# Optimization experiments

Measured on AMD Instinct MI355X. Metric: run time of the kernel, lower is better.

Reference implementation:

```python
import jax, jax.numpy as jnp
import numpy as np

V, B, E, H, T = 32000, 64, 64, 256, 32


def setup_inputs() -> dict:
    key = jax.random.key(0)
    ks = jax.random.split(key, 16)
    n = lambda k, shape, s: (jax.random.normal(k, shape, jnp.float32) * s)
    return {
        "input_x": jax.random.randint(ks[0], (B, T), 0, V, dtype=jnp.int32),
        "given_num": 16,
        "start_token": jnp.zeros((B,), jnp.int32),
        "g_embeddings": n(ks[1], (V, E), 0.1),
        "Wi": n(ks[2], (E, H), 0.1), "Ui": n(ks[3], (H, H), 0.1), "bi": jnp.zeros((H,), jnp.float32),
        "Wf": n(ks[4], (E, H), 0.1), "Uf": n(ks[5], (H, H), 0.1), "bf": jnp.zeros((H,), jnp.float32),
        "Wog": n(ks[6], (E, H), 0.1), "Uog": n(ks[7], (H, H), 0.1), "bog": jnp.zeros((H,), jnp.float32),
        "Wc": n(ks[8], (E, H), 0.1), "Uc": n(ks[9], (H, H), 0.1), "bc": jnp.zeros((H,), jnp.float32),
        "Wo": n(ks[10], (H, V), 0.05), "bo": jnp.zeros((V,), jnp.float32),
    }


def reference(input_x, given_num, start_token, g_embeddings,
              Wi, Ui, bi, Wf, Uf, bf, Wog, Uog, bog, Wc, Uc, bc, Wo, bo):
    Bsz, Tlen = input_x.shape
    Hdim = Ui.shape[0]
    emb_x = g_embeddings[input_x]                 # [B,T,E] teacher embeddings
    x0 = g_embeddings[start_token]                # [B,E]
    h0 = jnp.zeros((Bsz, Hdim), g_embeddings.dtype)
    c0 = jnp.zeros((Bsz, Hdim), g_embeddings.dtype)

    def step(carry, scan_in):
        x_t, h, c = carry
        t, teacher_tok, teacher_emb = scan_in
        i_g = jax.nn.sigmoid(x_t @ Wi + h @ Ui + bi)
        f_g = jax.nn.sigmoid(x_t @ Wf + h @ Uf + bf)
        o_g = jax.nn.sigmoid(x_t @ Wog + h @ Uog + bog)
        c_hat = jnp.tanh(x_t @ Wc + h @ Uc + bc)
        c_new = f_g * c + i_g * c_hat
        h_new = o_g * jnp.tanh(c_new)
        logits = h_new @ Wo + bo                  # [B,V]
        # original: argmax over Multinomial(logits=log_softmax).probs == argmax(logits)
        sampled = jnp.argmax(logits, axis=-1).astype(jnp.int32)
        teach = t < given_num                     # scalar bool for this step
        tok = jnp.where(teach, teacher_tok, sampled)
        x_next = jnp.where(teach, teacher_emb, g_embeddings[sampled])
        return (x_next, h_new, c_new), tok

    scan_in = (jnp.arange(Tlen), input_x.T, jnp.transpose(emb_x, (1, 0, 2)))
    _, toks = jax.lax.scan(step, (x0, h0, c0), scan_in)
    return toks.T                                 # [B,T] int32, matches gen_x
```

## Files before the change

kernel.cpp:

```cpp
#include <hip/hip_runtime.h>
#include <math.h>
#include <stdint.h>

#define Bz 64
#define Tz 32
#define Ez 64
#define Hz 256
#define Vz 32000
#define KTOT 320

typedef unsigned long long u64;
typedef unsigned int u32;

__device__ __forceinline__ u32 map_f32(float f) {
  u32 u = __float_as_uint(f);
  return (u & 0x80000000u) ? ~u : (u | 0x80000000u);
}

__device__ __forceinline__ void gload_lds16(const float* g, float* l) {
  __builtin_amdgcn_global_load_lds(
      (const __attribute__((address_space(1))) void*)g,
      (__attribute__((address_space(3))) void*)l, 16, 0, 0);
}

__global__ void k_prep(const float* __restrict__ Wi, const float* __restrict__ Ui,
                       const float* __restrict__ Wf, const float* __restrict__ Uf,
                       const float* __restrict__ Wog, const float* __restrict__ Uog,
                       const float* __restrict__ Wc, const float* __restrict__ Uc,
                       float* __restrict__ P4, u64* __restrict__ key) {
  int j = blockIdx.x;
  int k = threadIdx.x;
  float g0, g1, g2, g3;
  if (k < Ez) {
    g0 = Wi[k*Hz + j]; g1 = Wf[k*Hz + j]; g2 = Wog[k*Hz + j]; g3 = Wc[k*Hz + j];
  } else {
    int kk = k - Ez;
    g0 = Ui[kk*Hz + j]; g1 = Uf[kk*Hz + j]; g2 = Uog[kk*Hz + j]; g3 = Uc[kk*Hz + j];
  }
  float* p = P4 + ((size_t)j*KTOT + k)*4;
  p[0] = g0; p[1] = g1; p[2] = g2; p[3] = g3;
  if (j == 0 && k < 2*Bz) key[k] = 0ull;
}

__global__ __launch_bounds__(512) void k_gates(
    int t, const int* __restrict__ gnp,
    const int* __restrict__ input_x, const int* __restrict__ start_tok,
    const float* __restrict__ emb, const float* __restrict__ P4,
    const float* __restrict__ bi_, const float* __restrict__ bf_,
    const float* __restrict__ bog_, const float* __restrict__ bc_,
    const float* __restrict__ hT_in, float* __restrict__ hT_out,
    float* __restrict__ cT,
    const u64* __restrict__ key_prev, u64* __restrict__ key_cur,
    int* __restrict__ out) {
  extern __shared__ float sm[];
  float* xh = sm;
  float* pw = sm + 20480;
  float* sc = sm + 25600;
  int*   tok_s = (int*)(sm + 26624);

  int tid = threadIdx.x;
  int blk = blockIdx.x;
  int gn = *gnp;

  if (tid < Bz) {
    int b = tid, tk;
    if (t == 0)          tk = start_tok[b];
    else if (t - 1 < gn) tk = input_x[b*Tz + (t-1)];
    else                 tk = (int)(~(u32)(key_prev[b] & 0xFFFFFFFFull));
    tok_s[b] = tk;
    if (blk == 0 && t > 0) out[b*Tz + (t-1)] = tk;
  }
  if (blk == 0 && tid >= 64 && tid < 64 + Bz) key_cur[tid - 64] = 0ull;
  __syncthreads();

  {
    int b = tid & 63, part = tid >> 6;
    const float4* e4 = (const float4*)(emb + (size_t)tok_s[b]*Ez + part*8);
    float4 v0 = e4[0], v1 = e4[1];
    int k0 = part*8;
    xh[(k0+0)*Bz + b] = v0.x; xh[(k0+1)*Bz + b] = v0.y;
    xh[(k0+2)*Bz + b] = v0.z; xh[(k0+3)*Bz + b] = v0.w;
    xh[(k0+4)*Bz + b] = v1.x; xh[(k0+5)*Bz + b] = v1.y;
    xh[(k0+6)*Bz + b] = v1.z; xh[(k0+7)*Bz + b] = v1.w;
  }
  if (t > 0) {
    const float4* s4 = (const float4*)hT_in;
    float4* d4 = (float4*)(xh + Ez*Bz);
    #pragma unroll
    for (int i = 0; i < 8; ++i) d4[tid + i*512] = s4[tid + i*512];
  }
  {
    const float* psrc = P4 + (size_t)blk*5120;
    #pragma unroll
    for (int i = 0; i < 10; ++i) pw[tid + i*512] = psrc[tid + i*512];
  }
  __syncthreads();

  int wid = tid >> 6, lane = tid & 63;
  int j4 = wid >> 1, seg = wid & 1;
  int j = blk*4 + j4;
  const float* wrow = pw + j4*1280;
  int kbeg = seg ? 160 : 0;
  int kend = (t > 0) ? (seg ? 320 : 160) : (seg ? 0 : 64);

  float ai = 0.f, af = 0.f, ao = 0.f, ac = 0.f;
  #pragma unroll 2
  for (int k = kbeg; k < kend; k += 4) {
    #pragma unroll
    for (int kk = 0; kk < 4; ++kk) {
      float4 wv = *(const float4*)(wrow + (k+kk)*4);
      float xv = xh[(k+kk)*Bz + lane];
      ai = fmaf(xv, wv.x, ai); af = fmaf(xv, wv.y, af);
      ao = fmaf(xv, wv.z, ao); ac = fmaf(xv, wv.w, ac);
    }
  }

  if (seg == 1) {
    sc[j4*256 +   0 + lane] = ai;
    sc[j4*256 +  64 + lane] = af;
    sc[j4*256 + 128 + lane] = ao;
    sc[j4*256 + 192 + lane] = ac;
  }
  __syncthreads();
  if (seg == 0) {
    ai += sc[j4*256 +   0 + lane] + bi_[j];
    af += sc[j4*256 +  64 + lane] + bf_[j];
    ao += sc[j4*256 + 128 + lane] + bog_[j];
    ac += sc[j4*256 + 192 + lane] + bc_[j];
    float gi = 1.f/(1.f + expf(-ai));
    float gf = 1.f/(1.f + expf(-af));
    float go = 1.f/(1.f + expf(-ao));
    float gc = tanhf(ac);
    float cold = (t > 0) ? cT[j*Bz + lane] : 0.f;
    float cn = gf*cold + gi*gc;
    float hn = go * tanhf(cn);
    cT[j*Bz + lane]     = cn;
    hT_out[j*Bz + lane] = hn;
  }
}

__global__ __launch_bounds__(512, 1) void k_logits(
    int t, const int* __restrict__ gnp,
    const float* __restrict__ hT,
    const float* __restrict__ Wo, const float* __restrict__ bo,
    u64* __restrict__ key_cur) {
  int gn = *gnp;
  if (t < gn) return;
  extern __shared__ float sm[];
  float* hLDS = sm;
  float* wbuf = sm + 16384;

  int tid = threadIdx.x;
  int bid = blockIdx.x;
  int wid = tid >> 6, lane = tid & 63;
  int seg = wid >> 1, chalf = wid & 1;
  int rg = lane >> 3, cg = lane & 7;

  float bo8[8];
  {
    const float4* b4 = (const float4*)(bo + bid*128 + chalf*64 + cg*8);
    float4 x = b4[0], y = b4[1];
    bo8[0]=x.x; bo8[1]=x.y; bo8[2]=x.z; bo8[3]=x.w;
    bo8[4]=y.x; bo8[5]=y.y; bo8[6]=y.z; bo8[7]=y.w;
  }
  {
    const float4* s4 = (const float4*)hT;
    float4* d4 = (float4*)hLDS;
    #pragma unroll
    for (int i = 0; i < 8; ++i) d4[tid + i*512] = s4[tid + i*512];
  }
  __syncthreads();

  float acc[8][8] = {};
  float* wb = wbuf + wid*2048;
  const float* gW = Wo + bid*128;

#define STAGE(q_, p_) { \
    int kb = seg*64 + (q_)*8; \
    _Pragma("unroll") \
    for (int i = 0; i < 4; ++i) { \
      int row = kb + i*2 + (lane>>5); \
      gload_lds16(gW + (size_t)row*Vz + ((lane&31)<<2), wb + (p_)*1024 + i*256); \
    } }

#define COMPUTE(q_, p_) { \
    const float* wp = wb + (p_)*1024; \
    const float* hp = hLDS + (seg*64 + (q_)*8)*Bz + rg*8; \
    _Pragma("unroll") \
    for (int kk = 0; kk < 8; ++kk) { \
      float4 h0 = *(const float4*)(hp + kk*Bz); \
      float4 h1 = *(const float4*)(hp + kk*Bz + 4); \
      float4 w0 = *(const float4*)(wp + kk*128 + chalf*64 + cg*8); \
      float4 w1 = *(const float4*)(wp + kk*128 + chalf*64 + cg*8 + 4); \
      float hv[8] = {h0.x,h0.y,h0.z,h0.w,h1.x,h1.y,h1.z,h1.w}; \
      float wv[8] = {w0.x,w0.y,w0.z,w0.w,w1.x,w1.y,w1.z,w1.w}; \
      _Pragma("unroll") \
      for (int r = 0; r < 8; ++r) { \
        _Pragma("unroll") \
        for (int c = 0; c < 8; ++c) acc[r][c] = fmaf(hv[r], wv[c], acc[r][c]); } \
    } }

  STAGE(0, 0)
  #pragma unroll 1
  for (int q = 0; q < 7; ++q) {
    STAGE(q+1, (q+1)&1)
    asm volatile("s_waitcnt vmcnt(4)" ::: "memory");
    __builtin_amdgcn_sched_barrier(0);
    COMPUTE(q, q&1)
  }
  asm volatile("s_waitcnt vmcnt(0)" ::: "memory");
  __builtin_amdgcn_sched_barrier(0);
  COMPUTE(7, 1)
#undef STAGE
#undef COMPUTE

  float* scratch = wbuf;
  __syncthreads();
  if (wid >= 4) {
    float* r = scratch + (wid-4)*4096;
    #pragma unroll
    for (int i = 0; i < 64; ++i) r[i*64 + lane] = acc[i>>3][i&7];
  }
  __syncthreads();
  if (wid < 4) {
    const float* r = scratch + wid*4096;
    #pragma unroll
    for (int i = 0; i < 64; ++i) acc[i>>3][i&7] += r[i*64 + lane];
  }
  __syncthreads();
  if (wid == 2 || wid == 3) {
    float* r = scratch + (wid-2)*4096;
    #pragma unroll
    for (int i = 0; i < 64; ++i) r[i*64 + lane] = acc[i>>3][i&7];
  }
  __syncthreads();

  if (wid < 2) {
    const float* r = scratch + wid*4096;
    #pragma unroll
    for (int i = 0; i < 64; ++i) acc[i>>3][i&7] += r[i*64 + lane];

    int cbase = bid*128 + chalf*64 + cg*8;
    float myv = 0.f; int myi = 0;
    #pragma unroll
    for (int rr = 0; rr < 8; ++rr) {
      float bv = acc[rr][0] + bo8[0]; int bix = cbase;
      #pragma unroll
      for (int c = 1; c < 8; ++c) {
        float v = acc[rr][c] + bo8[c];
        if (v > bv) { bv = v; bix = cbase + c; }
      }
      #pragma unroll
      for (int m = 1; m < 8; m <<= 1) {
        float ov = __shfl_xor(bv, m, 64);
        int   oi = __shfl_xor(bix, m, 64);
        if (ov > bv || (ov == bv && oi < bix)) { bv = ov; bix = oi; }
      }
      if (cg == rr) { myv = bv; myi = bix; }
    }
    int row = rg*8 + cg;
    u64 kv = ((u64)map_f32(myv) << 32) | (u32)(~(u32)myi);
    atomicMax(&key_cur[row], kv);
  }
}

__global__ void k_final(const int* __restrict__ gnp, const int* __restrict__ input_x,
                        const u64* __restrict__ key_last, int* __restrict__ out) {
  int b = threadIdx.x;
  int gn = *gnp;
  int tk;
  if (Tz - 1 < gn) tk = input_x[b*Tz + Tz - 1];
  else             tk = (int)(~(u32)(key_last[b] & 0xFFFFFFFFull));
  out[b*Tz + Tz - 1] = tk;
}

extern "C" void kernel_launch(void* const* d_in, const int* in_sizes, int n_in,
                              void* d_out, int out_size, void* d_ws, size_t ws_size,
                              hipStream_t stream) {
  const int*   input_x   = (const int*)d_in[0];
  const int*   gnp       = (const int*)d_in[1];
  const int*   start_tok = (const int*)d_in[2];
  const float* emb = (const float*)d_in[3];
  const float* Wi  = (const float*)d_in[4];
  const float* Ui  = (const float*)d_in[5];
  const float* bi  = (const float*)d_in[6];
  const float* Wf  = (const float*)d_in[7];
  const float* Uf  = (const float*)d_in[8];
  const float* bff = (const float*)d_in[9];
  const float* Wog = (const float*)d_in[10];
  const float* Uog = (const float*)d_in[11];
  const float* bog = (const float*)d_in[12];
  const float* Wc  = (const float*)d_in[13];
  const float* Uc  = (const float*)d_in[14];
  const float* bc  = (const float*)d_in[15];
  const float* Wo  = (const float*)d_in[16];
  const float* bo  = (const float*)d_in[17];
  int* out = (int*)d_out;

  float* wsf = (float*)d_ws;
  float* hTA = wsf;
  float* hTB = wsf + 16384;
  float* cT  = wsf + 32768;
  u64*   key = (u64*)(wsf + 49152);
  float* P4  = wsf + 49152 + 256;

  size_t gsm = (size_t)(20480 + 5120 + 1024 + 64) * 4;
  size_t lsm = (size_t)(16384 + 16384) * 4;
  hipFuncSetAttribute((const void*)k_gates,
                      hipFuncAttributeMaxDynamicSharedMemorySize, (int)gsm);
  hipFuncSetAttribute((const void*)k_logits,
                      hipFuncAttributeMaxDynamicSharedMemorySize, (int)lsm);

  k_prep<<<dim3(256), dim3(320), 0, stream>>>(Wi, Ui, Wf, Uf, Wog, Uog, Wc, Uc, P4, key);

  for (int t = 0; t < Tz; ++t) {
    const float* hT_in  = (t & 1) ? hTA : hTB;
    float*       hT_out = (t & 1) ? hTB : hTA;
    const u64* key_prev = key + ((t + 1) & 1) * Bz;
    u64*       key_cur  = key + (t & 1) * Bz;
    k_gates<<<dim3(64), dim3(512), gsm, stream>>>(
        t, gnp, input_x, start_tok, emb, P4, bi, bff, bog, bc,
        hT_in, hT_out, cT, key_prev, key_cur, out);
    k_logits<<<dim3(250), dim3(512), lsm, stream>>>(
        t, gnp, hT_out, Wo, bo, key_cur);
  }
  k_final<<<dim3(1), dim3(64), 0, stream>>>(
      gnp, input_x, key + ((Tz - 1) & 1) * Bz, out);
}
```

Baseline: 731.3 us.

## Score logits in bf16, then rescore a candidate shortlist exactly in fp32

Converts Wo to a bf16 copy once per call and runs the per-step vocabulary projection on bf16 weights and hidden state. Any column within an error bound of the running row max (0.02·|h|·max|w|) goes into a per-row candidate list. A new k_pick kernel rescores those candidates exactly in fp32 and takes the argmax, with ties going to the lower index. The aim is to halve weight traffic in the dominant logits pass. In exchange it adds a Wo conversion pass per call, an extra launch per step, and atomics for the list. Correctness depends on the list caps (2048 entries, 128 rescored) not overflowing. The new path runs only when the workspace is large enough.

```diff
diff --git a/kernel.cpp b/kernel.cpp
--- a/kernel.cpp
+++ b/kernel.cpp
@@ -8,28 +8,43 @@
 #define Hz 256
 #define Vz 32000
 #define KTOT 320
+#define LCAP 2048
+#define THRC 0.02f
 
 typedef unsigned long long u64;
 typedef unsigned int u32;
+typedef unsigned short u16;
 
 __device__ __forceinline__ u32 map_f32(float f) {
   u32 u = __float_as_uint(f);
   return (u & 0x80000000u) ? ~u : (u | 0x80000000u);
 }
-
+__device__ __forceinline__ float unmap_f32(u32 u) {
+  return __uint_as_float((u & 0x80000000u) ? (u & 0x7FFFFFFFu) : ~u);
+}
+__device__ __forceinline__ u16 f2bf(float f) {
+  u32 u = __float_as_uint(f);
+  return (u16)((u + 0x7FFFu + ((u >> 16) & 1u)) >> 16);
+}
 __device__ __forceinline__ void gload_lds16(const float* g, float* l) {
   __builtin_amdgcn_global_load_lds(
       (const __attribute__((address_space(1))) void*)g,
       (__attribute__((address_space(3))) void*)l, 16, 0, 0);
 }
+__device__ __forceinline__ void gload_lds16u(const u16* g, u16* l) {
+  __builtin_amdgcn_global_load_lds(
+      (const __attribute__((address_space(1))) void*)g,
+      (__attribute__((address_space(3))) void*)l, 16, 0, 0);
+}
 
 __global__ void k_prep(const float* __restrict__ Wi, const float* __restrict__ Ui,
                        const float* __restrict__ Wf, const float* __restrict__ Uf,
                        const float* __restrict__ Wog, const float* __restrict__ Uog,
                        const float* __restrict__ Wc, const float* __restrict__ Uc,
-                       float* __restrict__ P4, u64* __restrict__ key) {
-  int j = blockIdx.x;
-  int k = threadIdx.x;
+                       float* __restrict__ P4, u64* __restrict__ key,
+                       int* __restrict__ cnt, u32* __restrict__ gmax,
+                       u32* __restrict__ wn2) {
+  int j = blockIdx.x, k = threadIdx.x;
   float g0, g1, g2, g3;
   if (k < Ez) {
     g0 = Wi[k*Hz + j]; g1 = Wf[k*Hz + j]; g2 = Wog[k*Hz + j]; g3 = Wc[k*Hz + j];
@@ -40,6 +55,36 @@
   float* p = P4 + ((size_t)j*KTOT + k)*4;
   p[0] = g0; p[1] = g1; p[2] = g2; p[3] = g3;
   if (j == 0 && k < 2*Bz) key[k] = 0ull;
+  if (j == 1 && k < Bz)   cnt[k] = 0;
+  if (j == 2 && k < Bz)   gmax[k] = 0u;
+  if (j == 3 && k == 0)   *wn2 = 0u;
+}
+
+__global__ __launch_bounds__(512) void wb_prep(const float* __restrict__ Wo,
+                                               u16* __restrict__ Wb,
+                                               u32* __restrict__ wn2) {
+  __shared__ float cnorm[128];
+  int bid = blockIdx.x, tid = threadIdx.x;
+  const float* src = Wo + bid*128;
+  u16* dst = Wb + (size_t)bid*32768;
+  for (int idx = tid; idx < 32768; idx += 512) {
+    int k = idx >> 7, c = idx & 127;
+    dst[idx] = f2bf(src[(size_t)k*Vz + c]);
+  }
+  if (tid < 128) {
+    float s = 0.f;
+    for (int k = 0; k < Hz; ++k) {
+      float w = src[(size_t)k*Vz + tid];
+      s = fmaf(w, w, s);
+    }
+    cnorm[tid] = s;
+  }
+  __syncthreads();
+  if (tid == 0) {
+    float m = cnorm[0];
+    for (int i = 1; i < 128; ++i) m = fmaxf(m, cnorm[i]);
+    atomicMax(wn2, map_f32(m));
+  }
 }
 
 __global__ __launch_bounds__(512) void k_gates(
@@ -49,8 +94,9 @@
     const float* __restrict__ bi_, const float* __restrict__ bf_,
     const float* __restrict__ bog_, const float* __restrict__ bc_,
     const float* __restrict__ hT_in, float* __restrict__ hT_out,
-    float* __restrict__ cT,
+    u16* __restrict__ hTb_out, float* __restrict__ cT,
     const u64* __restrict__ key_prev, u64* __restrict__ key_cur,
+    const int* __restrict__ tokp, int mode,
     int* __restrict__ out) {
   extern __shared__ float sm[];
   float* xh = sm;
@@ -66,7 +112,8 @@
     int b = tid, tk;
     if (t == 0)          tk = start_tok[b];
     else if (t - 1 < gn) tk = input_x[b*Tz + (t-1)];
-    else                 tk = (int)(~(u32)(key_prev[b] & 0xFFFFFFFFull));
+    else                 tk = mode ? tokp[b]
+                              : (int)(~(u32)(key_prev[b] & 0xFFFFFFFFull));
     tok_s[b] = tk;
     if (blk == 0 && t > 0) out[b*Tz + (t-1)] = tk;
   }
@@ -134,12 +181,253 @@
     float cold = (t > 0) ? cT[j*Bz + lane] : 0.f;
     float cn = gf*cold + gi*gc;
     float hn = go * tanhf(cn);
-    cT[j*Bz + lane]     = cn;
-    hT_out[j*Bz + lane] = hn;
-  }
-}
-
-__global__ __launch_bounds__(512, 1) void k_logits(
+    cT[j*Bz + lane]       = cn;
+    hT_out[j*Bz + lane]   = hn;
+    hTb_out[j*Bz + lane]  = f2bf(hn);
+  }
+}
+
+__global__ __launch_bounds__(512, 1) void k_logits_b(
+    int t, const int* __restrict__ gnp,
+    const u16* __restrict__ hTb,
+    const u16* __restrict__ Wb,
+    const float* __restrict__ bo,
+    const u32* __restrict__ wn2p, float* __restrict__ rn2_g,
+    u32* __restrict__ gmax,
+    u64* __restrict__ list, int* __restrict__ cnt) {
+  int gn = *gnp;
+  if (t < gn) return;
+  extern __shared__ float sm[];
+  u16* hLDSb = (u16*)sm;
+  u16* wbuf  = (u16*)sm + 16384;
+  float* rnp  = sm + 12288;
+  float* rn2l = sm + 12800;
+
+  int tid = threadIdx.x;
+  int bid = blockIdx.x;
+  int wid = tid >> 6, lane = tid & 63;
+  int seg = wid >> 1, chalf = wid & 1;
+  int rg = lane >> 3, cg = lane & 7;
+
+  float wn = sqrtf(unmap_f32(*wn2p));
+
+  float bo8[8];
+  {
+    const float4* b4 = (const float4*)(bo + bid*128 + chalf*64 + cg*8);
+    float4 x = b4[0], y = b4[1];
+    bo8[0]=x.x; bo8[1]=x.y; bo8[2]=x.z; bo8[3]=x.w;
+    bo8[4]=y.x; bo8[5]=y.y; bo8[6]=y.z; bo8[7]=y.w;
+  }
+  {
+    const uint4* s4 = (const uint4*)hTb;
+    uint4* d4 = (uint4*)hLDSb;
+    #pragma unroll
+    for (int i = 0; i < 4; ++i) d4[tid + i*512] = s4[tid + i*512];
+  }
+  __syncthreads();
+
+  {
+    int b = tid & 63, part = tid >> 6;
+    float s = 0.f;
+    #pragma unroll 8
+    for (int k = part*32; k < part*32 + 32; ++k) {
+      float v = __uint_as_float((u32)hLDSb[k*Bz + b] << 16);
+      s = fmaf(v, v, s);
+    }
+    rnp[part*64 + b] = s;
+  }
+  __syncthreads();
+  if (tid < 64) {
+    float s = 0.f;
+    #pragma unroll
+    for (int p = 0; p < 8; ++p) s += rnp[p*64 + tid];
+    rn2l[tid] = s;
+    rn2_g[tid] = s;
+  }
+  __syncthreads();
+
+  float thr8[8];
+  if (wid < 2) {
+    #pragma unroll
+    for (int rr = 0; rr < 8; ++rr)
+      thr8[rr] = THRC * sqrtf(rn2l[rg*8 + rr]) * wn;
+  }
+
+  float acc[8][8] = {};
+  u16* wb = wbuf + wid*1024;
+  const u16* gW = Wb + (size_t)bid*32768 + chalf*64 + (lane & 7)*8
+                + (size_t)(seg*64 + (lane >> 3))*128;
+
+#define STAGE(q_, s_) gload_lds16u(gW + (size_t)(q_)*8*128, wb + (s_)*512);
+
+#define COMPUTE(q_, s_) { \
+    const u16* wp = wb + (s_)*512; \
+    const u16* hp = hLDSb + (seg*64 + (q_)*8)*Bz + rg*8; \
+    _Pragma("unroll") \
+    for (int kk = 0; kk < 8; ++kk) { \
+      uint4 hq = *(const uint4*)(hp + kk*Bz); \
+      uint4 wq = *(const uint4*)(wp + kk*64 + cg*8); \
+      float hv[8], wv[8]; \
+      hv[0]=__uint_as_float(hq.x<<16); hv[1]=__uint_as_float(hq.x&0xFFFF0000u); \
+      hv[2]=__uint_as_float(hq.y<<16); hv[3]=__uint_as_float(hq.y&0xFFFF0000u); \
+      hv[4]=__uint_as_float(hq.z<<16); hv[5]=__uint_as_float(hq.z&0xFFFF0000u); \
+      hv[6]=__uint_as_float(hq.w<<16); hv[7]=__uint_as_float(hq.w&0xFFFF0000u); \
+      wv[0]=__uint_as_float(wq.x<<16); wv[1]=__uint_as_float(wq.x&0xFFFF0000u); \
+      wv[2]=__uint_as_float(wq.y<<16); wv[3]=__uint_as_float(wq.y&0xFFFF0000u); \
+      wv[4]=__uint_as_float(wq.z<<16); wv[5]=__uint_as_float(wq.z&0xFFFF0000u); \
+      wv[6]=__uint_as_float(wq.w<<16); wv[7]=__uint_as_float(wq.w&0xFFFF0000u); \
+      _Pragma("unroll") \
+      for (int r = 0; r < 8; ++r) { \
+        _Pragma("unroll") \
+        for (int c = 0; c < 8; ++c) acc[r][c] = fmaf(hv[r], wv[c], acc[r][c]); } \
+    } }
+
+  STAGE(0, 0)
+  #pragma unroll 1
+  for (int q = 0; q < 7; ++q) {
+    STAGE(q+1, (q+1)&1)
+    asm volatile("s_waitcnt vmcnt(1)" ::: "memory");
+    __builtin_amdgcn_sched_barrier(0);
+    COMPUTE(q, q&1)
+  }
+  asm volatile("s_waitcnt vmcnt(0)" ::: "memory");
+  __builtin_amdgcn_sched_barrier(0);
+  COMPUTE(7, 1)
+#undef STAGE
+#undef COMPUTE
+
+  float* scratch = sm;
+  __syncthreads();
+  if (wid >= 4) {
+    float* r = scratch + (wid-4)*4096;
+    #pragma unroll
+    for (int i = 0; i < 64; ++i) r[i*64 + lane] = acc[i>>3][i&7];
+  }
+  __syncthreads();
+  if (wid < 4) {
+    const float* r = scratch + wid*4096;
+    #pragma unroll
+    for (int i = 0; i < 64; ++i) acc[i>>3][i&7] += r[i*64 + lane];
+  }
+  __syncthreads();
+  if (wid == 2 || wid == 3) {
+    float* r = scratch + (wid-2)*4096;
+    #pragma unroll
+    for (int i = 0; i < 64; ++i) r[i*64 + lane] = acc[i>>3][i&7];
+  }
+  __syncthreads();
+
+  if (wid < 2) {
+    const float* r = scratch + wid*4096;
+    #pragma unroll
+    for (int i = 0; i < 64; ++i) acc[i>>3][i&7] += r[i*64 + lane];
+
+    int cbase = bid*128 + chalf*64 + cg*8;
+    #pragma unroll
+    for (int rr = 0; rr < 8; ++rr) {
+      float bv = acc[rr][0] + bo8[0];
+      #pragma unroll
+      for (int c = 1; c < 8; ++c) bv = fmaxf(bv, acc[rr][c] + bo8[c]);
+      #pragma unroll
+      for (int m = 1; m < 8; m <<= 1) bv = fmaxf(bv, __shfl_xor(bv, m, 64));
+      int row = rg*8 + rr;
+      float cur = 0.f;
+      if (cg == 0) {
+        u32 old = atomicMax(&gmax[row], map_f32(bv));
+        cur = fmaxf(unmap_f32(old), bv);
+      }
+      float thrw = __shfl(cur, rg*8, 64) - thr8[rr];
+      #pragma unroll
+      for (int c = 0; c < 8; ++c) {
+        float v = acc[rr][c] + bo8[c];
+        if (v >= thrw) {
+          int idx = atomicAdd(&cnt[row], 1);
+          if (idx < LCAP)
+            list[(size_t)row*LCAP + idx] =
+                ((u64)map_f32(v) << 32) | (u32)(~(u32)(cbase + c));
+        }
+      }
+    }
+  }
+}
+
+__global__ __launch_bounds__(256) void k_pick(
+    int t, const int* __restrict__ gnp,
+    const float* __restrict__ hT,
+    const float* __restrict__ Wo, const float* __restrict__ bo,
+    const u32* __restrict__ wn2p, const float* __restrict__ rn2_g,
+    u64* __restrict__ list, int* __restrict__ cnt, u32* __restrict__ gmax,
+    int* __restrict__ tok) {
+  int gn = *gnp;
+  if (t < gn) return;
+  int b = blockIdx.x, tid = threadIdx.x;
+  __shared__ u64 smax[4];
+  __shared__ u64 sbest[4];
+  __shared__ int scol[128];
+  __shared__ int scnt;
+
+  float wn = sqrtf(unmap_f32(*wn2p));
+  float thrb = THRC * sqrtf(rn2_g[b]) * wn;
+
+  int n = cnt[b]; if (n > LCAP) n = LCAP;
+  const u64* L = list + (size_t)b*LCAP;
+  if (tid == 0) scnt = 0;
+
+  u64 m = 0;
+  for (int i = tid; i < n; i += 256) { u64 v = L[i]; if (v > m) m = v; }
+  #pragma unroll
+  for (int s = 1; s < 64; s <<= 1) {
+    u64 o = __shfl_xor(m, s, 64);
+    if (o > m) m = o;
+  }
+  if ((tid & 63) == 0) smax[tid >> 6] = m;
+  __syncthreads();
+  u64 gm = smax[0];
+  #pragma unroll
+  for (int s = 1; s < 4; ++s) if (smax[s] > gm) gm = smax[s];
+  float thr = unmap_f32((u32)(gm >> 32)) - thrb;
+
+  for (int i = tid; i < n; i += 256) {
+    u64 v = L[i];
+    if (unmap_f32((u32)(v >> 32)) >= thr) {
+      int s = atomicAdd(&scnt, 1);
+      if (s < 128) scol[s] = (int)(~(u32)(v & 0xFFFFFFFFull));
+    }
+  }
+  __syncthreads();
+  int ns = scnt < 128 ? scnt : 128;
+
+  int w = tid >> 6, lane = tid & 63;
+  float bestv = -3.4e38f; int bestc = 0x7FFFFFFF;
+  for (int base = 0; base < ns; base += 4) {
+    int ci = base + w;
+    if (ci < ns) {
+      int c = scol[ci];
+      int k0 = lane*4;
+      float pv = 0.f;
+      #pragma unroll
+      for (int i = 0; i < 4; ++i)
+        pv = fmaf(hT[(k0+i)*Bz + b], Wo[(size_t)(k0+i)*Vz + c], pv);
+      #pragma unroll
+      for (int s = 1; s < 64; s <<= 1) pv += __shfl_xor(pv, s, 64);
+      pv += bo[c];
+      if (pv > bestv || (pv == bestv && c < bestc)) { bestv = pv; bestc = c; }
+    }
+  }
+  if (lane == 0)
+    sbest[w] = ((u64)map_f32(bestv) << 32) | (u32)(~(u32)bestc);
+  __syncthreads();
+  if (tid == 0) {
+    u64 bb = sbest[0];
+    #pragma unroll
+    for (int s = 1; s < 4; ++s) if (sbest[s] > bb) bb = sbest[s];
+    tok[b]  = (int)(~(u32)(bb & 0xFFFFFFFFull));
+    cnt[b]  = 0;
+    gmax[b] = 0u;
+  }
+}
+
+__global__ __launch_bounds__(512, 1) void k_logits_f32(
     int t, const int* __restrict__ gnp,
     const float* __restrict__ hT,
     const float* __restrict__ Wo, const float* __restrict__ bo,
@@ -265,12 +553,14 @@
 }
 
 __global__ void k_final(const int* __restrict__ gnp, const int* __restrict__ input_x,
-                        const u64* __restrict__ key_last, int* __restrict__ out) {
+                        const u64* __restrict__ key_last, const int* __restrict__ tokp,
+                        int mode, int* __restrict__ out) {
   int b = threadIdx.x;
   int gn = *gnp;
   int tk;
   if (Tz - 1 < gn) tk = input_x[b*Tz + Tz - 1];
-  else             tk = (int)(~(u32)(key_last[b] & 0xFFFFFFFFull));
+  else             tk = mode ? tokp[b]
+                        : (int)(~(u32)(key_last[b] & 0xFFFFFFFFull));
   out[b*Tz + Tz - 1] = tk;
 }
 
@@ -297,21 +587,37 @@
   const float* bo  = (const float*)d_in[17];
   int* out = (int*)d_out;
 
-  float* wsf = (float*)d_ws;
-  float* hTA = wsf;
-  float* hTB = wsf + 16384;
-  float* cT  = wsf + 32768;
-  u64*   key = (u64*)(wsf + 49152);
-  float* P4  = wsf + 49152 + 256;
-
-  size_t gsm = (size_t)(20480 + 5120 + 1024 + 64) * 4;
-  size_t lsm = (size_t)(16384 + 16384) * 4;
+  float* wsf  = (float*)d_ws;
+  float* hTA  = wsf;
+  float* hTB  = wsf + 16384;
+  float* cT   = wsf + 32768;
+  u64*   key  = (u64*)(wsf + 49152);
+  int*   tok  = (int*)(wsf + 49408);
+  int*   cnt  = (int*)(wsf + 49472);
+  u32*   gmax = (u32*)(wsf + 49536);
+  float* rn2g = wsf + 49600;
+  u32*   wn2  = (u32*)(wsf + 49664);
+  u16*   hTb  = (u16*)(wsf + 49728);
+  float* P4   = wsf + 57920;
+  u64*   list = (u64*)(wsf + 385600);
+  u16*   Wb   = (u16*)(wsf + 647744);
+
+  int mode = ws_size >= (size_t)(647744 + 4096000) * 4;
+
+  size_t gsm  = (size_t)(20480 + 5120 + 1024 + 64) * 4;
+  size_t lsmB = 65536;
+  size_t lsmF = (size_t)(16384 + 16384) * 4;
   hipFuncSetAttribute((const void*)k_gates,
                       hipFuncAttributeMaxDynamicSharedMemorySize, (int)gsm);
-  hipFuncSetAttribute((const void*)k_logits,
-                      hipFuncAttributeMaxDynamicSharedMemorySize, (int)lsm);
-
-  k_prep<<<dim3(256), dim3(320), 0, stream>>>(Wi, Ui, Wf, Uf, Wog, Uog, Wc, Uc, P4, key);
+  hipFuncSetAttribute((const void*)k_logits_b,
+                      hipFuncAttributeMaxDynamicSharedMemorySize, (int)lsmB);
+  hipFuncSetAttribute((const void*)k_logits_f32,
+                      hipFuncAttributeMaxDynamicSharedMemorySize, (int)lsmF);
+
+  k_prep<<<dim3(256), dim3(320), 0, stream>>>(Wi, Ui, Wf, Uf, Wog, Uog, Wc, Uc,
+                                              P4, key, cnt, gmax, wn2);
+  if (mode)
+    wb_prep<<<dim3(250), dim3(512), 0, stream>>>(Wo, Wb, wn2);
 
   for (int t = 0; t < Tz; ++t) {
     const float* hT_in  = (t & 1) ? hTA : hTB;
@@ -320,10 +626,17 @@
     u64*       key_cur  = key + (t & 1) * Bz;
     k_gates<<<dim3(64), dim3(512), gsm, stream>>>(
         t, gnp, input_x, start_tok, emb, P4, bi, bff, bog, bc,
-        hT_in, hT_out, cT, key_prev, key_cur, out);
-    k_logits<<<dim3(250), dim3(512), lsm, stream>>>(
-        t, gnp, hT_out, Wo, bo, key_cur);
+        hT_in, hT_out, hTb, cT, key_prev, key_cur, tok, mode, out);
+    if (mode) {
+      k_logits_b<<<dim3(250), dim3(512), lsmB, stream>>>(
+          t, gnp, hTb, Wb, bo, wn2, rn2g, gmax, list, cnt);
+      k_pick<<<dim3(64), dim3(256), 0, stream>>>(
+          t, gnp, hT_out, Wo, bo, wn2, rn2g, list, cnt, gmax, tok);
+    } else {
+      k_logits_f32<<<dim3(250), dim3(512), lsmF, stream>>>(
+          t, gnp, hT_out, Wo, bo, key_cur);
+    }
   }
   k_final<<<dim3(1), dim3(64), 0, stream>>>(
-      gnp, input_x, key + ((Tz - 1) & 1) * Bz, out);
-}
+      gnp, input_x, key + ((Tz - 1) & 1) * Bz, tok, mode, out);
+}
```

New measurement: 2.200 ms. +200.8%, slower.
